# Optimization experiments

Hardware: AMD Instinct MI355X
Metric: run time of the kernel (lower is better)

## Reference

```python
import jax, jax.numpy as jnp
import numpy as np

N = 10000
E = 320000
D = 256
EPS = 1e-5

def layer_norm(x, g, b):
    mu = jnp.mean(x, axis=-1, keepdims=True)
    var = jnp.mean(jnp.square(x - mu), axis=-1, keepdims=True)
    return (x - mu) * jax.lax.rsqrt(var + EPS) * g + b

def linear(x, w, b):
    # w: [in, out]
    return x @ w + b

def setup_inputs() -> dict:
    key = jax.random.key(0)
    ks = jax.random.split(key, 20)
    s = 1.0 / np.sqrt(D)
    inp = {
        'x': jax.random.normal(ks[0], (N, D), jnp.float32),
        'edge_index': jax.random.randint(ks[1], (2, E), 0, N, jnp.int64),
        'edge_weight': jax.random.normal(ks[2], (E,), jnp.float32),
        'wq': jax.random.normal(ks[3], (D, D), jnp.float32) * s,
        'bq': jnp.zeros((D,), jnp.float32),
        'wk': jax.random.normal(ks[4], (D, D), jnp.float32) * s,
        'bk': jnp.zeros((D,), jnp.float32),
        'wv': jax.random.normal(ks[5], (D, D), jnp.float32) * s,
        'bv': jnp.zeros((D,), jnp.float32),
        'ws': jax.random.normal(ks[6], (D, D), jnp.float32) * s,
        'bs': jnp.zeros((D,), jnp.float32),
        'we': jax.random.normal(ks[7], (1, 1), jnp.float32),
        'be': jnp.zeros((1,), jnp.float32),
        'g1': jnp.ones((D,), jnp.float32),
        'b1': jnp.zeros((D,), jnp.float32),
        'g2': jnp.ones((D,), jnp.float32),
        'b2': jnp.zeros((D,), jnp.float32),
        'w_ff1': jax.random.normal(ks[8], (D, 2 * D), jnp.float32) * s,
        'b_ff1': jnp.zeros((2 * D,), jnp.float32),
        'w_ff2': jax.random.normal(ks[9], (2 * D, D), jnp.float32) * (1.0 / np.sqrt(2 * D)),
        'b_ff2': jnp.zeros((D,), jnp.float32),
    }
    return inp

def reference(x, edge_index, edge_weight, wq, bq, wk, bk, wv, bv, ws, bs, we, be,
              g1, b1, g2, b2, w_ff1, b_ff1, w_ff2, b_ff2):
    n = x.shape[0]
    scale = x.shape[-1] ** (-0.5)
    q = linear(x, wq, bq)
    k = linear(x, wk, bk)
    v = linear(x, wv, bv)
    src, dst = edge_index[0], edge_index[1]
    # per-edge attention scores: dot(q[dst], k[src]) * scale
    scores = jnp.sum(q[dst] * k[src], axis=-1) * scale
    scores = scores + (edge_weight[:, None] @ we + be)[:, 0]
    # two-pass segment softmax over dst
    seg_max = jax.ops.segment_max(scores, dst, num_segments=n)
    exp_s = jnp.exp(scores - seg_max[dst])
    denom = jax.ops.segment_sum(exp_s, dst, num_segments=n)
    attn = exp_s / jnp.maximum(denom[dst], 1e-12)
    # scatter-add weighted messages
    message = v[src] * attn[:, None]  # [E, D]
    out = jax.ops.segment_sum(message, dst, num_segments=n)
    x = layer_norm(x + out + linear(x, ws, bs), g1, b1)
    ffn = linear(jax.nn.gelu(linear(x, w_ff1, b_ff1)), w_ff2, b_ff2)
    x = layer_norm(x + ffn, g2, b2)
    return x
```

## Files before the change

### kernel.cpp

```cpp
#include <hip/hip_runtime.h>
#include <math.h>

#define N_NODES 10000
#define N_EDGES 320000
#define DIM 256
#define BCAP 128

#define P_PARTS 250
#define NPP 40
#define PCAP 2048
#define EPT 16

typedef __attribute__((ext_vector_type(8))) short bf16x8;
typedef __attribute__((ext_vector_type(4))) float fx4;

typedef __attribute__((address_space(3))) unsigned lds_u32;
typedef __attribute__((address_space(1))) const unsigned gbl_u32;


__device__ __forceinline__ float gelu_tanh(float x) {
  const float k0 = 0.7978845608028654f;
  float x3 = x * x * x;
  return 0.5f * x * (1.0f + tanhf(k0 * (x + 0.044715f * x3)));
}

__device__ __forceinline__ unsigned short f2bf(float f) {
  unsigned u = __float_as_uint(f);
  unsigned r = 0x7FFFu + ((u >> 16) & 1u);
  return (unsigned short)((u + r) >> 16);
}

__device__ __forceinline__ float bf_lo(unsigned u) { return __uint_as_float(u << 16); }
__device__ __forceinline__ float bf_hi(unsigned u) { return __uint_as_float(u & 0xFFFF0000u); }


#define SEG_QKVS 262144
#define SEG_FF1 131072
#define SEG_FF2 131072
#define SEG_BIAS 1024
#define SEG_CONV 320000
#define SEG_ZCNT 256
#define PREP_TOTAL (SEG_QKVS + SEG_FF1 + SEG_FF2 + SEG_BIAS + SEG_CONV + SEG_ZCNT)

__global__ __launch_bounds__(256) void prep_all_kernel(
    const float* __restrict__ wq, const float* __restrict__ wk,
    const float* __restrict__ wv, const float* __restrict__ ws,
    const float* __restrict__ bq, const float* __restrict__ bk,
    const float* __restrict__ bv, const float* __restrict__ bs,
    const float* __restrict__ wff1, const float* __restrict__ wff2,
    const float* __restrict__ x,
    unsigned short* __restrict__ wt_qkvs, float* __restrict__ bias_qkvs,
    unsigned short* __restrict__ wt_ff1, unsigned short* __restrict__ wt_ff2,
    unsigned short* __restrict__ xb, unsigned* __restrict__ pcnt) {
  int id = blockIdx.x * 256 + threadIdx.x;
  if (id < SEG_QKVS) {
    const int n = id >> 8, k = id & 255;
    const float* w = (n < 256) ? wq : (n < 512) ? wk : (n < 768) ? wv : ws;
    wt_qkvs[id] = f2bf(w[k * 256 + (n & 255)]);
    return;
  }
  id -= SEG_QKVS;
  if (id < SEG_FF1) {
    const int n = id >> 8, k = id & 255;
    wt_ff1[id] = f2bf(wff1[k * 512 + n]);
    return;
  }
  id -= SEG_FF1;
  if (id < SEG_FF2) {
    const int n = id >> 9, k = id & 511;
    wt_ff2[id] = f2bf(wff2[k * 256 + n]);
    return;
  }
  id -= SEG_FF2;
  if (id < SEG_BIAS) {
    bias_qkvs[id] = (id < 256) ? bq[id] : (id < 512) ? bk[id & 255]
                    : (id < 768) ? bv[id & 255] : bs[id & 255];
    return;
  }
  id -= SEG_BIAS;
  if (id < SEG_CONV) {
    const int base = id * 8;
    float4 a = *(const float4*)(x + base);
    float4 b = *(const float4*)(x + base + 4);
    unsigned short h[8] = {f2bf(a.x), f2bf(a.y), f2bf(a.z), f2bf(a.w),
                           f2bf(b.x), f2bf(b.y), f2bf(b.z), f2bf(b.w)};
    *(uint4*)(xb + base) = *(const uint4*)h;
    return;
  }
  id -= SEG_CONV;
  if (id < SEG_ZCNT) pcnt[id] = 0u;
}

__global__ __launch_bounds__(512) void scatter_p1(
    const int* __restrict__ ei, const float* __restrict__ ew,
    const float* __restrict__ we, const float* __restrict__ be,
    unsigned* __restrict__ pcnt, uint2* __restrict__ pbuf) {
  __shared__ unsigned lcnt[P_PARTS];
  __shared__ unsigned lbase[P_PARTS];
  const int tid = threadIdx.x;
  for (int i = tid; i < P_PARTS; i += 512) lcnt[i] = 0;
  __syncthreads();
  const float wes = we[0], bes = be[0];
  const int e0 = blockIdx.x * (512 * EPT);

  unsigned pp[EPT];
  unsigned rr[EPT];
  unsigned sv[EPT];
  float ebv[EPT];
#pragma unroll
  for (int j = 0; j < EPT; j++) {
    const int e = e0 + j * 512 + tid;
    pp[j] = 0;
    rr[j] = 0xFFFFFFFFu;
    if (e < N_EDGES) {
      const int dst = ei[N_EDGES + e];
      const int src = ei[e];
      const int p = dst / NPP;
      sv[j] = (unsigned)dst | ((unsigned)src << 16);
      ebv[j] = fmaf(ew[e], wes, bes);
      pp[j] = (unsigned)p;
      rr[j] = atomicAdd(&lcnt[p], 1u);
    }
  }
  __syncthreads();
  for (int i = tid; i < P_PARTS; i += 512) {
    const unsigned c = lcnt[i];
    lbase[i] = c ? atomicAdd(&pcnt[i], c) : 0u;
  }
  __syncthreads();
#pragma unroll
  for (int j = 0; j < EPT; j++) {
    if (rr[j] != 0xFFFFFFFFu) {
      const unsigned pos = lbase[pp[j]] + rr[j];
      if (pos < PCAP) {
        uint2 rec;
        rec.x = sv[j];
        rec.y = __float_as_uint(ebv[j]);
        pbuf[(size_t)pp[j] * PCAP + pos] = rec;
      }
    }
  }
}

__global__ __launch_bounds__(256) void scatter_p2(
    const unsigned* __restrict__ pcnt, const uint2* __restrict__ pbuf,
    unsigned* __restrict__ cnt, uint2* __restrict__ es_csr) {
  __shared__ unsigned lcnt[NPP];
  const int p = blockIdx.x;
  const int tid = threadIdx.x;
  if (tid < NPP) lcnt[tid] = 0;
  __syncthreads();
  const int n0 = p * NPP;
  const int tot = min((int)pcnt[p], PCAP);
  for (int i = tid; i < tot; i += 256) {
    const uint2 rec = pbuf[(size_t)p * PCAP + i];
    const int dst = (int)(rec.x & 0xFFFFu);
    const int src = (int)(rec.x >> 16);
    const unsigned r = atomicAdd(&lcnt[dst - n0], 1u);
    if (r < BCAP) {
      uint2 o;
      o.x = (unsigned)src;
      o.y = rec.y;
      es_csr[(size_t)dst * BCAP + r] = o;
    }
  }
  __syncthreads();
  if (tid < NPP) cnt[n0 + tid] = lcnt[tid];
}

template <int GELU, int WF32, int WB16, int SPLIT>
__global__ __launch_bounds__(256) void mfma_gemm(
    const unsigned short* __restrict__ A, int lda,
    const unsigned short* __restrict__ Bt,
    const float* __restrict__ bias,
    const float* __restrict__ xres,
    float* __restrict__ C, int ldc,
    unsigned short* __restrict__ Cb, int ldcb,
    int M, int K) {
  __shared__ char lds[32768];
  const int tid = threadIdx.x;

  const int l = tid & 63;
  const int wid = tid >> 6;
  const int wrow = (wid & 1) * 32;
  const int wcol = (wid >> 1) * 32;
  const int bm = blockIdx.y * 64;
  const int bn = blockIdx.x * 64;

  fx4 acc[2][2];
#pragma unroll
  for (int i = 0; i < 2; i++)
#pragma unroll
    for (int j = 0; j < 2; j++) acc[i][j] = (fx4)(0.0f);

#define STAGE(BUFOFF, KB)                                                      \
  {                                                                            \
    _Pragma("unroll") for (int i = 0; i < 2; i++) {                            \
      const int id = i * 256 + tid;                                            \
      const int row = id >> 3;                                                 \
      const int ccs = (id & 7) ^ (row & 7);                                    \
      __builtin_amdgcn_global_load_lds(                                        \
          (gbl_u32*)(A + (size_t)(bm + row) * lda + (KB) + ccs * 8),           \
          (lds_u32*)(lds + (BUFOFF) + id * 16), 16, 0, 0);                     \
    }                                                                          \
    _Pragma("unroll") for (int i = 0; i < 2; i++) {                            \
      const int id = i * 256 + tid;                                            \
      const int row = id >> 3;                                                 \
      const int ccs = (id & 7) ^ (row & 7);                                    \
      __builtin_amdgcn_global_load_lds(                                        \
          (gbl_u32*)(Bt + (size_t)(bn + row) * K + (KB) + ccs * 8),            \
          (lds_u32*)(lds + (BUFOFF) + 8192 + id * 16), 16, 0, 0);              \
    }                                                                          \
  }

  STAGE(0, 0);

  unsigned cur = 0;
  for (int kb = 0; kb < K; kb += 64) {
    if (kb + 64 < K) {
      STAGE((cur ^ 1) * 16384, kb + 64);
      asm volatile("s_waitcnt vmcnt(4)" ::: "memory");
    } else {
      asm volatile("s_waitcnt vmcnt(0)" ::: "memory");
    }
    __builtin_amdgcn_s_barrier();
    __builtin_amdgcn_sched_barrier(0);

    const char* As = lds + cur * 16384;
    const char* Bs = As + 8192;
#pragma unroll
    for (int kk = 0; kk < 2; kk++) {
      const int kbyte = (kk * 64 + ((l >> 4) << 4)) ^ ((l & 7) << 4);
      bf16x8 af[2], bg[2];
#pragma unroll
      for (int f = 0; f < 2; f++) {
        const int ar = wrow + f * 16 + (l & 15);
        af[f] = *(const bf16x8*)(As + ar * 128 + kbyte);
        const int br = wcol + f * 16 + (l & 15);
        bg[f] = *(const bf16x8*)(Bs + br * 128 + kbyte);
      }
#pragma unroll
      for (int fr = 0; fr < 2; fr++)
#pragma unroll
        for (int fc = 0; fc < 2; fc++)
          acc[fr][fc] = __builtin_amdgcn_mfma_f32_16x16x32_bf16(
              bg[fc], af[fr], acc[fr][fc], 0, 0, 0);
    }
    __builtin_amdgcn_s_barrier();
    cur ^= 1;
  }
#undef STAGE

#pragma unroll
  for (int fr = 0; fr < 2; fr++) {
    const int m = bm + wrow + fr * 16 + (l & 15);
    if (m < M) {
#pragma unroll
      for (int fc = 0; fc < 2; fc++) {
        const int n0 = bn + wcol + fc * 16 + ((l >> 4) << 2);
        const float4 b4 = *(const float4*)(bias + n0);
        fx4 v = acc[fr][fc];
        float o0 = v[0] + b4.x;
        float o1 = v[1] + b4.y;
        float o2 = v[2] + b4.z;
        float o3 = v[3] + b4.w;
        if (GELU) {
          o0 = gelu_tanh(o0); o1 = gelu_tanh(o1);
          o2 = gelu_tanh(o2); o3 = gelu_tanh(o3);
        }
        if (SPLIT) {
          const int seg = n0 >> 8, nn = n0 & 255;
          if (seg == 3) {
            const float4 xr = *(const float4*)(xres + (size_t)m * 256 + nn);
            float4 w;
            w.x = o0 + xr.x; w.y = o1 + xr.y; w.z = o2 + xr.z; w.w = o3 + xr.w;
            *(float4*)(C + (size_t)m * 256 + nn) = w;
          } else {
            uint2 pk;
            pk.x = (unsigned)f2bf(o0) | ((unsigned)f2bf(o1) << 16);
            pk.y = (unsigned)f2bf(o2) | ((unsigned)f2bf(o3) << 16);
            *(uint2*)(Cb + (size_t)seg * (N_NODES * DIM) + (size_t)m * 256 + nn) = pk;
          }
        } else {
          if (WF32) {
            float4 w; w.x = o0; w.y = o1; w.z = o2; w.w = o3;
            *(float4*)(C + (size_t)m * ldc + n0) = w;
          }
          if (WB16) {
            uint2 pk;
            pk.x = (unsigned)f2bf(o0) | ((unsigned)f2bf(o1) << 16);
            pk.y = (unsigned)f2bf(o2) | ((unsigned)f2bf(o3) << 16);
            *(uint2*)(Cb + (size_t)m * ldcb + n0) = pk;
          }
        }
      }
    }
  }
}

__global__ __launch_bounds__(256) void ffn_fused(
    const unsigned short* __restrict__ x1b,
    const unsigned short* __restrict__ w1,
    const float* __restrict__ b1,
    const unsigned short* __restrict__ w2,
    const float* __restrict__ b2,
    float* __restrict__ y, int M) {
  __shared__ char hlds[16 * 1024];
  const int tid = threadIdx.x;
  const int l = tid & 63;
  const int wv = tid >> 6;
  const int bm = blockIdx.x * 16;
  const int ml = l & 15;
  const int kc = l >> 4;
  const int swz = (ml & 7) << 4;

  uint4 af[8];
  {
    const unsigned short* ar = x1b + (size_t)(bm + ml) * 256 + kc * 8;
#pragma unroll
    for (int kk = 0; kk < 8; kk++) af[kk] = *(const uint4*)(ar + kk * 32);
  }

#pragma unroll
  for (int cf = 0; cf < 8; cf++) {
    const int nb = wv * 128 + cf * 16;
    const unsigned short* br = w1 + (size_t)(nb + ml) * 256 + kc * 8;
    fx4 acc = (fx4)(0.0f);
#pragma unroll
    for (int kk = 0; kk < 8; kk++) {
      const uint4 bv = *(const uint4*)(br + kk * 32);
      acc = __builtin_amdgcn_mfma_f32_16x16x32_bf16(
          *(const bf16x8*)(&bv), *(const bf16x8*)(&af[kk]), acc, 0, 0, 0);
    }
    const int n0 = nb + kc * 4;
    const float4 b4 = *(const float4*)(b1 + n0);
    const float o0 = gelu_tanh(acc[0] + b4.x);
    const float o1 = gelu_tanh(acc[1] + b4.y);
    const float o2 = gelu_tanh(acc[2] + b4.z);
    const float o3 = gelu_tanh(acc[3] + b4.w);
    uint2 pk;
    pk.x = (unsigned)f2bf(o0) | ((unsigned)f2bf(o1) << 16);
    pk.y = (unsigned)f2bf(o2) | ((unsigned)f2bf(o3) << 16);
    *(uint2*)(hlds + ml * 1024 + ((n0 * 2) ^ swz)) = pk;
  }
  __syncthreads();

  fx4 acc2[4];
#pragma unroll
  for (int cf = 0; cf < 4; cf++) acc2[cf] = (fx4)(0.0f);
#pragma unroll
  for (int kk = 0; kk < 16; kk++) {
    const bf16x8 a = *(const bf16x8*)(
        hlds + ml * 1024 + (((kc * 16) + kk * 64) ^ swz));
#pragma unroll
    for (int cf = 0; cf < 4; cf++) {
      const int n = wv * 64 + cf * 16 + ml;
      const uint4 bv = *(const uint4*)(w2 + (size_t)n * 512 + kc * 8 + kk * 32);
      acc2[cf] = __builtin_amdgcn_mfma_f32_16x16x32_bf16(
          *(const bf16x8*)(&bv), a, acc2[cf], 0, 0, 0);
    }
  }
  const int m = bm + ml;
  if (m >= M) return;
#pragma unroll
  for (int cf = 0; cf < 4; cf++) {
    const int n0 = wv * 64 + cf * 16 + kc * 4;
    const float4 b4 = *(const float4*)(b2 + n0);
    float4 o;
    o.x = acc2[cf][0] + b4.x;
    o.y = acc2[cf][1] + b4.y;
    o.z = acc2[cf][2] + b4.z;
    o.w = acc2[cf][3] + b4.w;
    *(float4*)(y + (size_t)m * 256 + n0) = o;
  }
}

__global__ __launch_bounds__(64) void agg_fused_kernel(
    const unsigned* __restrict__ cnt, const uint2* __restrict__ es_csr,
    const unsigned short* __restrict__ qb,
    const unsigned short* __restrict__ kb, const unsigned short* __restrict__ vb,
    const float* __restrict__ sbuf,
    const float* __restrict__ g, const float* __restrict__ b,
    float* __restrict__ out, unsigned short* __restrict__ outb) {
  const int node = blockIdx.x;
  const int lane = threadIdx.x;
  const int grp = lane >> 4;
  const int t = lane & 15;
  const int start = node * BCAP;
  const int deg = min((int)cnt[node], BCAP);
  const int end = start + deg;

  const uint4 qA = *(const uint4*)(qb + (size_t)node * 256 + t * 16);
  const uint4 qB = *(const uint4*)(qb + (size_t)node * 256 + t * 16 + 8);
  float qf[16];
  qf[0] = bf_lo(qA.x);  qf[1] = bf_hi(qA.x);
  qf[2] = bf_lo(qA.y);  qf[3] = bf_hi(qA.y);
  qf[4] = bf_lo(qA.z);  qf[5] = bf_hi(qA.z);
  qf[6] = bf_lo(qA.w);  qf[7] = bf_hi(qA.w);
  qf[8] = bf_lo(qB.x);  qf[9] = bf_hi(qB.x);
  qf[10] = bf_lo(qB.y); qf[11] = bf_hi(qB.y);
  qf[12] = bf_lo(qB.z); qf[13] = bf_hi(qB.z);
  qf[14] = bf_lo(qB.w); qf[15] = bf_hi(qB.w);

  float m = -3.4e38f, dsum = 0.f;
  float a0 = 0.f, a1 = 0.f, a2 = 0.f, a3 = 0.f;

  int ea = start + grp * 2;
  int eb_ = ea + 1;
  bool va = ea < end, vbd = eb_ < end;
  int sa = 0, sb = 0;
  float ba = 0.f, bb = 0.f;
  if (va) { const uint2 es = es_csr[ea]; sa = (int)es.x; ba = __uint_as_float(es.y); }
  if (vbd) { const uint2 es = es_csr[eb_]; sb = (int)es.x; bb = __uint_as_float(es.y); }
  uint4 kAa = *(const uint4*)(kb + (size_t)sa * 256 + t * 16);
  uint4 kBa = *(const uint4*)(kb + (size_t)sa * 256 + t * 16 + 8);
  uint4 kAb = *(const uint4*)(kb + (size_t)sb * 256 + t * 16);
  uint4 kBb = *(const uint4*)(kb + (size_t)sb * 256 + t * 16 + 8);

  for (int base = start; base < end; base += 8) {
    const int s0 = __shfl(sa, 0), s1 = __shfl(sa, 16);
    const int s2 = __shfl(sa, 32), s3 = __shfl(sa, 48);
    const int s4 = __shfl(sb, 0), s5 = __shfl(sb, 16);
    const int s6 = __shfl(sb, 32), s7 = __shfl(sb, 48);
    const uint2 v0 = *(const uint2*)(vb + (size_t)s0 * 256 + lane * 4);
    const uint2 v1 = *(const uint2*)(vb + (size_t)s1 * 256 + lane * 4);
    const uint2 v2 = *(const uint2*)(vb + (size_t)s2 * 256 + lane * 4);
    const uint2 v3 = *(const uint2*)(vb + (size_t)s3 * 256 + lane * 4);
    const uint2 v4 = *(const uint2*)(vb + (size_t)s4 * 256 + lane * 4);
    const uint2 v5 = *(const uint2*)(vb + (size_t)s5 * 256 + lane * 4);
    const uint2 v6 = *(const uint2*)(vb + (size_t)s6 * 256 + lane * 4);
    const uint2 v7 = *(const uint2*)(vb + (size_t)s7 * 256 + lane * 4);

    const int na = base + 8 + grp * 2;
    const int nb = na + 1;
    const bool va_n = na < end, vb_n = nb < end;
    int sa_n = 0, sb_n = 0;
    float ba_n = 0.f, bb_n = 0.f;
    if (va_n) { const uint2 es = es_csr[na]; sa_n = (int)es.x; ba_n = __uint_as_float(es.y); }
    if (vb_n) { const uint2 es = es_csr[nb]; sb_n = (int)es.x; bb_n = __uint_as_float(es.y); }

    float da = qf[0] * bf_lo(kAa.x);
    float db = qf[0] * bf_lo(kAb.x);
    da = fmaf(qf[1], bf_hi(kAa.x), da);  db = fmaf(qf[1], bf_hi(kAb.x), db);
    da = fmaf(qf[2], bf_lo(kAa.y), da);  db = fmaf(qf[2], bf_lo(kAb.y), db);
    da = fmaf(qf[3], bf_hi(kAa.y), da);  db = fmaf(qf[3], bf_hi(kAb.y), db);
    da = fmaf(qf[4], bf_lo(kAa.z), da);  db = fmaf(qf[4], bf_lo(kAb.z), db);
    da = fmaf(qf[5], bf_hi(kAa.z), da);  db = fmaf(qf[5], bf_hi(kAb.z), db);
    da = fmaf(qf[6], bf_lo(kAa.w), da);  db = fmaf(qf[6], bf_lo(kAb.w), db);
    da = fmaf(qf[7], bf_hi(kAa.w), da);  db = fmaf(qf[7], bf_hi(kAb.w), db);
    da = fmaf(qf[8], bf_lo(kBa.x), da);  db = fmaf(qf[8], bf_lo(kBb.x), db);
    da = fmaf(qf[9], bf_hi(kBa.x), da);  db = fmaf(qf[9], bf_hi(kBb.x), db);
    da = fmaf(qf[10], bf_lo(kBa.y), da); db = fmaf(qf[10], bf_lo(kBb.y), db);
    da = fmaf(qf[11], bf_hi(kBa.y), da); db = fmaf(qf[11], bf_hi(kBb.y), db);
    da = fmaf(qf[12], bf_lo(kBa.z), da); db = fmaf(qf[12], bf_lo(kBb.z), db);
    da = fmaf(qf[13], bf_hi(kBa.z), da); db = fmaf(qf[13], bf_hi(kBb.z), db);
    da = fmaf(qf[14], bf_lo(kBa.w), da); db = fmaf(qf[14], bf_lo(kBb.w), db);
    da = fmaf(qf[15], bf_hi(kBa.w), da); db = fmaf(qf[15], bf_hi(kBb.w), db);
    da += __shfl_xor(da, 1);  db += __shfl_xor(db, 1);
    da += __shfl_xor(da, 2);  db += __shfl_xor(db, 2);
    da += __shfl_xor(da, 4);  db += __shfl_xor(db, 4);
    da += __shfl_xor(da, 8);  db += __shfl_xor(db, 8);
    const float sca = va ? fmaf(da, 0.0625f, ba) : -3.4e38f;
    const float scb = vbd ? fmaf(db, 0.0625f, bb) : -3.4e38f;

    const uint4 kAa_n = *(const uint4*)(kb + (size_t)sa_n * 256 + t * 16);
    const uint4 kBa_n = *(const uint4*)(kb + (size_t)sa_n * 256 + t * 16 + 8);
    const uint4 kAb_n = *(const uint4*)(kb + (size_t)sb_n * 256 + t * 16);
    const uint4 kBb_n = *(const uint4*)(kb + (size_t)sb_n * 256 + t * 16 + 8);

    const float c0 = __shfl(sca, 0), c1 = __shfl(sca, 16);
    const float c2 = __shfl(sca, 32), c3 = __shfl(sca, 48);
    const float c4 = __shfl(scb, 0), c5 = __shfl(scb, 16);
    const float c6 = __shfl(scb, 32), c7 = __shfl(scb, 48);

    const float mx = fmaxf(fmaxf(fmaxf(c0, c1), fmaxf(c2, c3)),
                           fmaxf(fmaxf(c4, c5), fmaxf(c6, c7)));
    const float mn = fmaxf(m, mx);
    const float scale = __expf(m - mn);
    const float w0 = __expf(c0 - mn), w1 = __expf(c1 - mn);
    const float w2 = __expf(c2 - mn), w3 = __expf(c3 - mn);
    const float w4 = __expf(c4 - mn), w5 = __expf(c5 - mn);
    const float w6 = __expf(c6 - mn), w7 = __expf(c7 - mn);
    dsum = fmaf(dsum, scale, ((w0 + w1) + (w2 + w3)) + ((w4 + w5) + (w6 + w7)));

    float t0 = a0 * scale;
    t0 = fmaf(w0, bf_lo(v0.x), t0); t0 = fmaf(w1, bf_lo(v1.x), t0);
    t0 = fmaf(w2, bf_lo(v2.x), t0); t0 = fmaf(w3, bf_lo(v3.x), t0);
    t0 = fmaf(w4, bf_lo(v4.x), t0); t0 = fmaf(w5, bf_lo(v5.x), t0);
    t0 = fmaf(w6, bf_lo(v6.x), t0); t0 = fmaf(w7, bf_lo(v7.x), t0);
    a0 = t0;
    float t1 = a1 * scale;
    t1 = fmaf(w0, bf_hi(v0.x), t1); t1 = fmaf(w1, bf_hi(v1.x), t1);
    t1 = fmaf(w2, bf_hi(v2.x), t1); t1 = fmaf(w3, bf_hi(v3.x), t1);
    t1 = fmaf(w4, bf_hi(v4.x), t1); t1 = fmaf(w5, bf_hi(v5.x), t1);
    t1 = fmaf(w6, bf_hi(v6.x), t1); t1 = fmaf(w7, bf_hi(v7.x), t1);
    a1 = t1;
    float t2 = a2 * scale;
    t2 = fmaf(w0, bf_lo(v0.y), t2); t2 = fmaf(w1, bf_lo(v1.y), t2);
    t2 = fmaf(w2, bf_lo(v2.y), t2); t2 = fmaf(w3, bf_lo(v3.y), t2);
    t2 = fmaf(w4, bf_lo(v4.y), t2); t2 = fmaf(w5, bf_lo(v5.y), t2);
    t2 = fmaf(w6, bf_lo(v6.y), t2); t2 = fmaf(w7, bf_lo(v7.y), t2);
    a2 = t2;
    float t3 = a3 * scale;
    t3 = fmaf(w0, bf_hi(v0.y), t3); t3 = fmaf(w1, bf_hi(v1.y), t3);
    t3 = fmaf(w2, bf_hi(v2.y), t3); t3 = fmaf(w3, bf_hi(v3.y), t3);
    t3 = fmaf(w4, bf_hi(v4.y), t3); t3 = fmaf(w5, bf_hi(v5.y), t3);
    t3 = fmaf(w6, bf_hi(v6.y), t3); t3 = fmaf(w7, bf_hi(v7.y), t3);
    a3 = t3;
    m = mn;

    sa = sa_n; sb = sb_n;
    ba = ba_n; bb = bb_n;
    va = va_n; vbd = vb_n;
    kAa = kAa_n; kBa = kBa_n;
    kAb = kAb_n; kBb = kBb_n;
  }
  const float inv = 1.0f / fmaxf(dsum, 1e-12f);

  const float4 sv = *(const float4*)(sbuf + (size_t)node * 256 + lane * 4);
  float r0 = a0 * inv + sv.x;
  float r1 = a1 * inv + sv.y;
  float r2 = a2 * inv + sv.z;
  float r3 = a3 * inv + sv.w;

  float sum = r0 + r1 + r2 + r3;
#pragma unroll
  for (int off = 32; off > 0; off >>= 1) sum += __shfl_xor(sum, off);
  const float mu = sum * (1.0f / 256.0f);
  const float d0 = r0 - mu, d1 = r1 - mu, d2 = r2 - mu, d3 = r3 - mu;
  float vs = d0 * d0 + d1 * d1 + d2 * d2 + d3 * d3;
#pragma unroll
  for (int off = 32; off > 0; off >>= 1) vs += __shfl_xor(vs, off);
  const float rs = rsqrtf(vs * (1.0f / 256.0f) + 1e-5f);

  const float4 gv = *(const float4*)(g + lane * 4);
  const float4 bv = *(const float4*)(b + lane * 4);
  float4 o;
  o.x = d0 * rs * gv.x + bv.x;
  o.y = d1 * rs * gv.y + bv.y;
  o.z = d2 * rs * gv.z + bv.z;
  o.w = d3 * rs * gv.w + bv.w;
  *(float4*)(out + (size_t)node * 256 + lane * 4) = o;
  uint2 pk;
  pk.x = (unsigned)f2bf(o.x) | ((unsigned)f2bf(o.y) << 16);
  pk.y = (unsigned)f2bf(o.z) | ((unsigned)f2bf(o.w) << 16);
  *(uint2*)(outb + (size_t)node * 256 + lane * 4) = pk;
}


__global__ __launch_bounds__(256) void ln2_kernel(
    const float* __restrict__ x1, const float* __restrict__ y,
    const float* __restrict__ g, const float* __restrict__ b,
    float* __restrict__ out) {
  __shared__ float red[4];
  const int row = blockIdx.x;
  const int t = threadIdx.x;
  const size_t idx = (size_t)row * 256 + t;
  float v = x1[idx] + y[idx];
  float s = v;
#pragma unroll
  for (int off = 32; off > 0; off >>= 1) s += __shfl_xor(s, off);
  if ((t & 63) == 0) red[t >> 6] = s;
  __syncthreads();
  float tot = red[0] + red[1] + red[2] + red[3];
  __syncthreads();
  const float mu = tot * (1.0f / 256.0f);
  const float d = v - mu;
  float vs = d * d;
#pragma unroll
  for (int off = 32; off > 0; off >>= 1) vs += __shfl_xor(vs, off);
  if ((t & 63) == 0) red[t >> 6] = vs;
  __syncthreads();
  float vtot = red[0] + red[1] + red[2] + red[3];
  const float r = rsqrtf(vtot * (1.0f / 256.0f) + 1e-5f);
  out[idx] = d * r * g[t] + b[t];
}


extern "C" void kernel_launch(void* const* d_in, const int* in_sizes, int n_in,
                              void* d_out, int out_size, void* d_ws,
                              size_t ws_size, hipStream_t stream) {
  const float* x = (const float*)d_in[0];
  const int* ei = (const int*)d_in[1];
  const float* ew = (const float*)d_in[2];
  const float* wq = (const float*)d_in[3];
  const float* bq = (const float*)d_in[4];
  const float* wk = (const float*)d_in[5];
  const float* bk = (const float*)d_in[6];
  const float* wv = (const float*)d_in[7];
  const float* bv = (const float*)d_in[8];
  const float* wsm = (const float*)d_in[9];
  const float* bs = (const float*)d_in[10];
  const float* we = (const float*)d_in[11];
  const float* be = (const float*)d_in[12];
  const float* g1 = (const float*)d_in[13];
  const float* b1 = (const float*)d_in[14];
  const float* g2 = (const float*)d_in[15];
  const float* b2 = (const float*)d_in[16];
  const float* wff1 = (const float*)d_in[17];
  const float* bff1 = (const float*)d_in[18];
  const float* wff2 = (const float*)d_in[19];
  const float* bff2 = (const float*)d_in[20];
  float* out = (float*)d_out;

  unsigned short* qb = (unsigned short*)d_ws;
  unsigned short* kbp = qb + 2560000;
  unsigned short* vbp = qb + 5120000;
  float* sbuf = (float*)(qb + 7680000);
  uint2* es_csr = (uint2*)(sbuf + 2560000);
  unsigned* cnt = (unsigned*)(es_csr + (size_t)N_NODES * BCAP);
  float* x1 = (float*)(cnt + N_NODES);
  float* y = x1 + 2560000;
  unsigned short* x1b = (unsigned short*)(y + 2560000);
  unsigned short* h_b = x1b + 2560000;
  unsigned short* xb = h_b;
  unsigned short* wt_qkvs = h_b + 5120000;
  unsigned short* wt_ff1 = wt_qkvs + 262144;
  unsigned short* wt_ff2 = wt_ff1 + 131072;
  float* bias_qkvs = (float*)(wt_ff2 + 131072);
  unsigned* pcnt = (unsigned*)(bias_qkvs + 1024);
  uint2* pbuf = (uint2*)(pcnt + 256);

  dim3 blk(256);
  const int mb = (N_NODES + 63) / 64;

  prep_all_kernel<<<(PREP_TOTAL + 255) / 256, blk, 0, stream>>>(
      wq, wk, wv, wsm, bq, bk, bv, bs, wff1, wff2, x,
      wt_qkvs, bias_qkvs, wt_ff1, wt_ff2, xb, pcnt);

  scatter_p1<<<(N_EDGES + 512 * EPT - 1) / (512 * EPT), dim3(512), 0, stream>>>(
      ei, ew, we, be, pcnt, pbuf);
  scatter_p2<<<P_PARTS, blk, 0, stream>>>(pcnt, pbuf, cnt, es_csr);

  mfma_gemm<0, 0, 0, 1><<<dim3(16, mb), blk, 0, stream>>>(
      xb, 256, wt_qkvs, bias_qkvs, x, sbuf, 0, qb, 0, N_NODES, 256);

  agg_fused_kernel<<<N_NODES, dim3(64), 0, stream>>>(
      cnt, es_csr, qb, kbp, vbp, sbuf, g1, b1, x1, x1b);

  ffn_fused<<<dim3((N_NODES + 15) / 16), blk, 0, stream>>>(
      x1b, wt_ff1, bff1, wt_ff2, bff2, y, N_NODES);

  ln2_kernel<<<N_NODES, blk, 0, stream>>>(x1, y, g2, b2, out);
}
```

Before: 145.7 us.

## Fuse second LayerNorm into FFN kernel with 512-thread blocks

Merges the FFN kernel and the final residual+LayerNorm kernel into one. The intermediate y buffer no longer makes a global round trip, and one launch is removed. Blocks grow to 512 threads (8 waves) so each 16-row tile is covered by twice as many waves, each doing half the columns. Row statistics are reduced through shared memory. The LDS XOR swizzle is replaced by a padded 1040-byte row stride, which trades one bank-conflict avoidance scheme for another. The M bounds check is dropped, which is safe because N is divisible by 16.

```diff
diff --git a/kernel.cpp b/kernel.cpp
--- a/kernel.cpp
+++ b/kernel.cpp
@@ -298,21 +298,24 @@
   }
 }
 
-__global__ __launch_bounds__(256) void ffn_fused(
+__global__ __launch_bounds__(512) void ffn_ln_fused(
     const unsigned short* __restrict__ x1b,
+    const float* __restrict__ x1,
     const unsigned short* __restrict__ w1,
     const float* __restrict__ b1,
     const unsigned short* __restrict__ w2,
     const float* __restrict__ b2,
-    float* __restrict__ y, int M) {
-  __shared__ char hlds[16 * 1024];
+    const float* __restrict__ g, const float* __restrict__ bln,
+    float* __restrict__ out) {
+  __shared__ char hlds[16 * 1040];
+  __shared__ float red1[128];
+  __shared__ float red2[128];
   const int tid = threadIdx.x;
   const int l = tid & 63;
   const int wv = tid >> 6;
   const int bm = blockIdx.x * 16;
   const int ml = l & 15;
   const int kc = l >> 4;
-  const int swz = (ml & 7) << 4;
 
   uint4 af[8];
   {
@@ -322,8 +325,8 @@
   }
 
 #pragma unroll
-  for (int cf = 0; cf < 8; cf++) {
-    const int nb = wv * 128 + cf * 16;
+  for (int cf = 0; cf < 4; cf++) {
+    const int nb = wv * 64 + cf * 16;
     const unsigned short* br = w1 + (size_t)(nb + ml) * 256 + kc * 8;
     fx4 acc = (fx4)(0.0f);
 #pragma unroll
@@ -341,37 +344,72 @@
     uint2 pk;
     pk.x = (unsigned)f2bf(o0) | ((unsigned)f2bf(o1) << 16);
     pk.y = (unsigned)f2bf(o2) | ((unsigned)f2bf(o3) << 16);
-    *(uint2*)(hlds + ml * 1024 + ((n0 * 2) ^ swz)) = pk;
-  }
-  __syncthreads();
-
-  fx4 acc2[4];
-#pragma unroll
-  for (int cf = 0; cf < 4; cf++) acc2[cf] = (fx4)(0.0f);
+    *(uint2*)(hlds + ml * 1040 + n0 * 2) = pk;
+  }
+  __syncthreads();
+
+  fx4 acc2[2];
+  acc2[0] = (fx4)(0.0f);
+  acc2[1] = (fx4)(0.0f);
 #pragma unroll
   for (int kk = 0; kk < 16; kk++) {
-    const bf16x8 a = *(const bf16x8*)(
-        hlds + ml * 1024 + (((kc * 16) + kk * 64) ^ swz));
-#pragma unroll
-    for (int cf = 0; cf < 4; cf++) {
-      const int n = wv * 64 + cf * 16 + ml;
+    const bf16x8 a = *(const bf16x8*)(hlds + ml * 1040 + kc * 16 + kk * 64);
+#pragma unroll
+    for (int cf = 0; cf < 2; cf++) {
+      const int n = wv * 32 + cf * 16 + ml;
       const uint4 bv = *(const uint4*)(w2 + (size_t)n * 512 + kc * 8 + kk * 32);
       acc2[cf] = __builtin_amdgcn_mfma_f32_16x16x32_bf16(
           *(const bf16x8*)(&bv), a, acc2[cf], 0, 0, 0);
     }
   }
+
   const int m = bm + ml;
-  if (m >= M) return;
-#pragma unroll
-  for (int cf = 0; cf < 4; cf++) {
-    const int n0 = wv * 64 + cf * 16 + kc * 4;
+  float r[8];
+  float s = 0.f;
+#pragma unroll
+  for (int cf = 0; cf < 2; cf++) {
+    const int n0 = wv * 32 + cf * 16 + kc * 4;
     const float4 b4 = *(const float4*)(b2 + n0);
+    const float4 x4 = *(const float4*)(x1 + (size_t)m * 256 + n0);
+    r[cf * 4 + 0] = acc2[cf][0] + b4.x + x4.x;
+    r[cf * 4 + 1] = acc2[cf][1] + b4.y + x4.y;
+    r[cf * 4 + 2] = acc2[cf][2] + b4.z + x4.z;
+    r[cf * 4 + 3] = acc2[cf][3] + b4.w + x4.w;
+    s += (r[cf * 4 + 0] + r[cf * 4 + 1]) + (r[cf * 4 + 2] + r[cf * 4 + 3]);
+  }
+  s += __shfl_xor(s, 16);
+  s += __shfl_xor(s, 32);
+  if (kc == 0) red1[wv * 16 + ml] = s;
+  __syncthreads();
+  float tot = 0.f;
+#pragma unroll
+  for (int wi = 0; wi < 8; wi++) tot += red1[wi * 16 + ml];
+  const float mu = tot * (1.0f / 256.0f);
+  float vsum = 0.f;
+#pragma unroll
+  for (int j = 0; j < 8; j++) {
+    const float d = r[j] - mu;
+    vsum += d * d;
+  }
+  vsum += __shfl_xor(vsum, 16);
+  vsum += __shfl_xor(vsum, 32);
+  if (kc == 0) red2[wv * 16 + ml] = vsum;
+  __syncthreads();
+  float vtot = 0.f;
+#pragma unroll
+  for (int wi = 0; wi < 8; wi++) vtot += red2[wi * 16 + ml];
+  const float rs = rsqrtf(vtot * (1.0f / 256.0f) + 1e-5f);
+#pragma unroll
+  for (int cf = 0; cf < 2; cf++) {
+    const int n0 = wv * 32 + cf * 16 + kc * 4;
+    const float4 g4 = *(const float4*)(g + n0);
+    const float4 bb4 = *(const float4*)(bln + n0);
     float4 o;
-    o.x = acc2[cf][0] + b4.x;
-    o.y = acc2[cf][1] + b4.y;
-    o.z = acc2[cf][2] + b4.z;
-    o.w = acc2[cf][3] + b4.w;
-    *(float4*)(y + (size_t)m * 256 + n0) = o;
+    o.x = (r[cf * 4 + 0] - mu) * rs * g4.x + bb4.x;
+    o.y = (r[cf * 4 + 1] - mu) * rs * g4.y + bb4.y;
+    o.z = (r[cf * 4 + 2] - mu) * rs * g4.z + bb4.z;
+    o.w = (r[cf * 4 + 3] - mu) * rs * g4.w + bb4.w;
+    *(float4*)(out + (size_t)m * 256 + n0) = o;
   }
 }
 
@@ -548,35 +586,6 @@
 }
 
 
-__global__ __launch_bounds__(256) void ln2_kernel(
-    const float* __restrict__ x1, const float* __restrict__ y,
-    const float* __restrict__ g, const float* __restrict__ b,
-    float* __restrict__ out) {
-  __shared__ float red[4];
-  const int row = blockIdx.x;
-  const int t = threadIdx.x;
-  const size_t idx = (size_t)row * 256 + t;
-  float v = x1[idx] + y[idx];
-  float s = v;
-#pragma unroll
-  for (int off = 32; off > 0; off >>= 1) s += __shfl_xor(s, off);
-  if ((t & 63) == 0) red[t >> 6] = s;
-  __syncthreads();
-  float tot = red[0] + red[1] + red[2] + red[3];
-  __syncthreads();
-  const float mu = tot * (1.0f / 256.0f);
-  const float d = v - mu;
-  float vs = d * d;
-#pragma unroll
-  for (int off = 32; off > 0; off >>= 1) vs += __shfl_xor(vs, off);
-  if ((t & 63) == 0) red[t >> 6] = vs;
-  __syncthreads();
-  float vtot = red[0] + red[1] + red[2] + red[3];
-  const float r = rsqrtf(vtot * (1.0f / 256.0f) + 1e-5f);
-  out[idx] = d * r * g[t] + b[t];
-}
-
-
 extern "C" void kernel_launch(void* const* d_in, const int* in_sizes, int n_in,
                               void* d_out, int out_size, void* d_ws,
                               size_t ws_size, hipStream_t stream) {
@@ -638,8 +647,6 @@
   agg_fused_kernel<<<N_NODES, dim3(64), 0, stream>>>(
       cnt, es_csr, qb, kbp, vbp, sbuf, g1, b1, x1, x1b);
 
-  ffn_fused<<<dim3((N_NODES + 15) / 16), blk, 0, stream>>>(
-      x1b, wt_ff1, bff1, wt_ff2, bff2, y, N_NODES);
-
-  ln2_kernel<<<N_NODES, blk, 0, stream>>>(x1, y, g2, b2, out);
-}
+  ffn_ln_fused<<<dim3(625), dim3(512), 0, stream>>>(
+      x1b, x1, wt_ff1, bff1, wt_ff2, bff2, g2, b2, out);
+}
```

Result: faster. 141.5 us (-2.9%).
